# Kernel optimization log

Hardware: AMD Instinct MI355X
Metric: run time of the kernel (lower is better)

Reference implementation:

```python
import jax, jax.numpy as jnp
import numpy as np

D_MODEL = 128; D_STATE = 64; HEADDIM = 32; D_CONV = 4; EXPAND = 2
D_INNER = EXPAND * D_MODEL          # 256
NHEADS = D_INNER // HEADDIM         # 8
NGROUPS = 1
D_CONV_CH = D_INNER + 2 * NGROUPS * D_STATE      # 384
D_IN_PROJ = 2 * D_INNER + 2 * NGROUPS * D_STATE + NHEADS  # 648


def _mamba2(u, Win, convw, convb, dtb, Alog, Dp, normw, Wout):
    # u: (B, L, d_model). Mamba2 forward (ngroups=1, rmsnorm gated, no in/out bias).
    B, L, _ = u.shape
    zxbcdt = u @ Win                                   # (B,L,648)
    z, xBC, dt = jnp.split(zxbcdt, [D_INNER, D_INNER + D_CONV_CH], axis=-1)
    # depthwise causal conv1d (kernel D_CONV) + SiLU
    xp = jnp.pad(xBC, ((0, 0), (D_CONV - 1, 0), (0, 0)))
    xconv = sum(xp[:, k:k + L, :] * convw[k] for k in range(D_CONV)) + convb
    xBC = jax.nn.silu(xconv)
    x, Bm, Cm = jnp.split(xBC, [D_INNER, D_INNER + NGROUPS * D_STATE], axis=-1)
    dt = jax.nn.softplus(dt + dtb)                     # (B,L,H)
    A = -jnp.exp(Alog)                                 # (H,)
    xh = x.reshape(B, L, NHEADS, HEADDIM)              # (B,L,H,P)
    dA = jnp.exp(dt * A)                               # (B,L,H)

    def step(h, inp):
        dA_t, dt_t, B_t, C_t, x_t = inp
        h = h * dA_t[:, :, None, None] + jnp.einsum('bh,bn,bhp->bhpn', dt_t, B_t, x_t)
        y = jnp.einsum('bhpn,bn->bhp', h, C_t)
        return h, y

    h0 = jnp.zeros((B, NHEADS, HEADDIM, D_STATE), dtype=u.dtype)
    xs = (jnp.moveaxis(dA, 1, 0), jnp.moveaxis(dt, 1, 0), jnp.moveaxis(Bm, 1, 0),
          jnp.moveaxis(Cm, 1, 0), jnp.moveaxis(xh, 1, 0))
    _, ys = jax.lax.scan(step, h0, xs)
    y = jnp.moveaxis(ys, 0, 1) + Dp[None, None, :, None] * xh   # skip D
    y = y.reshape(B, L, D_INNER)
    # RMSNormGated (norm_before_gate=False): rmsnorm(y * silu(z)) * weight
    y = y * jax.nn.silu(z)
    y = y * jax.lax.rsqrt(jnp.mean(y * y, axis=-1, keepdims=True) + 1e-5) * normw
    return y @ Wout


def _cross_attn(x, ctx, Wq, bq, Wk, bk, Wv, bv, Wo, bo):
    Q = x @ Wq + bq
    K = ctx @ Wk + bk
    V = ctx @ Wv + bv
    att = jax.nn.softmax(jnp.einsum('bqd,bkd->bqk', Q, K) * (D_MODEL ** -0.5), axis=-1)
    return jnp.einsum('bqk,bkd->bqd', att, V) @ Wo + bo


def setup_inputs() -> dict:
    key = jax.random.key(0)
    ks = jax.random.split(key, 8)
    B, L = 2048, 8

    def lin(k, fi, fo):
        return jax.random.normal(k, (fi, fo), jnp.float32) / np.sqrt(fi)

    def mamba_params(kseq):
        k = jax.random.split(kseq, 6)
        dt = jax.random.uniform(k[3], (NHEADS,), minval=0.001, maxval=0.1)
        return {
            'Win': lin(k[0], D_MODEL, D_IN_PROJ),
            'convw': jax.random.normal(k[1], (D_CONV, D_CONV_CH), jnp.float32) * 0.2,
            'convb': jnp.zeros((D_CONV_CH,), jnp.float32),
            'dtb': dt + jnp.log(-jnp.expm1(-dt)),  # inverse softplus
            'Alog': jnp.log(jax.random.uniform(k[4], (NHEADS,), minval=1.0, maxval=16.0)),
            'D': jnp.ones((NHEADS,), jnp.float32),
            'normw': jnp.ones((D_INNER,), jnp.float32),
            'Wout': lin(k[5], D_INNER, D_MODEL),
        }

    inp = {
        'st_feature': jax.random.normal(ks[0], (B, L, D_MODEL), jnp.float32),
        'exp_feature': jax.random.normal(ks[1], (B, L, D_MODEL), jnp.float32),
    }
    for pref, p in (('st_', mamba_params(ks[2])), ('ex_', mamba_params(ks[3]))):
        for n, v in p.items():
            inp[pref + n] = v

    def ca(kseq, pref):
        k = jax.random.split(kseq, 4)
        d = {}
        for n, kk in zip(('Wq', 'Wk', 'Wv', 'Wo'), k):
            d[pref + n] = lin(kk, D_MODEL, D_MODEL)
            d[pref + 'b' + n[1]] = jnp.zeros((D_MODEL,), jnp.float32)
        return d

    inp.update(ca(ks[4], 'cx_'))  # cross_atten_exp
    inp.update(ca(ks[5], 'cs_'))  # cross_atten_st
    inp['mlp_W'] = lin(ks[6], 8 * 2 * D_MODEL, 1024)
    inp['mlp_b'] = jnp.zeros((1024,), jnp.float32)
    return inp


def reference(st_feature, exp_feature,
              st_Win, st_convw, st_convb, st_dtb, st_Alog, st_D, st_normw, st_Wout,
              ex_Win, ex_convw, ex_convb, ex_dtb, ex_Alog, ex_D, ex_normw, ex_Wout,
              cx_Wq, cx_bq, cx_Wk, cx_bk, cx_Wv, cx_bv, cx_Wo, cx_bo,
              cs_Wq, cs_bq, cs_Wk, cs_bk, cs_Wv, cs_bv, cs_Wo, cs_bo,
              mlp_W, mlp_b):
    exp_f = _mamba2(exp_feature, ex_Win, ex_convw, ex_convb, ex_dtb, ex_Alog, ex_D, ex_normw, ex_Wout)
    st_f = _mamba2(st_feature, st_Win, st_convw, st_convb, st_dtb, st_Alog, st_D, st_normw, st_Wout)
    exp_a = _cross_attn(exp_f, st_f, cx_Wq, cx_bq, cx_Wk, cx_bk, cx_Wv, cx_bv, cx_Wo, cx_bo)
    st_a = _cross_attn(st_f, exp_f, cs_Wq, cs_bq, cs_Wk, cs_bk, cs_Wv, cs_bv, cs_Wo, cs_bo)
    x = jnp.concatenate([st_a, exp_a], axis=-1)        # (B, 8, 256)
    x = x.reshape(x.shape[0], -1)                      # (B, 2048)
    return x @ mlp_W + mlp_b
```

## Files before the change

kernel.cpp:

```cpp
#include <hip/hip_runtime.h>
#include <hip/hip_bf16.h>
#include <math.h>

#define B_SZ 2048
#define L_SEQ 8
#define DMODEL 128
#define DSTATE 64
#define HEADDIM 32
#define DCONV 4
#define DINNER 256
#define NHEADS 8
#define DCONVCH 384
#define DINPROJ 648
#define NPAD 656

typedef short bf16x8 __attribute__((ext_vector_type(8)));
typedef float floatx4 __attribute__((ext_vector_type(4)));

__device__ __forceinline__ float siluf(float x) {
    return x / (1.f + expf(-x));
}
__device__ __forceinline__ float bf2f(unsigned short h) {
    unsigned int u = ((unsigned int)h) << 16;
    return __builtin_bit_cast(float, u);
}
__device__ __forceinline__ unsigned short f2bf(float f) {
    __hip_bfloat16 b = __float2bfloat16(f);
    return __builtin_bit_cast(unsigned short, b);
}
__device__ __forceinline__ void unpack8(bf16x8 v, float* o) {
    #pragma unroll
    for (int j = 0; j < 8; ++j) o[j] = bf2f((unsigned short)v[j]);
}
__device__ __forceinline__ void gl_lds16(const unsigned short* g, unsigned short* l) {
    __builtin_amdgcn_global_load_lds(
        (const __attribute__((address_space(1))) unsigned int*)g,
        (__attribute__((address_space(3))) unsigned int*)l, 16, 0, 0);
}

__global__ __launch_bounds__(256) void prep_weights(
    const float* __restrict__ st_Win, const float* __restrict__ ex_Win,
    const float* __restrict__ st_Wout, const float* __restrict__ ex_Wout,
    const float* __restrict__ cs_Wq, const float* __restrict__ cs_Wk,
    const float* __restrict__ cs_Wv, const float* __restrict__ cs_Wo,
    const float* __restrict__ cx_Wq, const float* __restrict__ cx_Wk,
    const float* __restrict__ cx_Wv, const float* __restrict__ cx_Wo,
    const float* __restrict__ mlp_W,
    unsigned short* __restrict__ winT_st, unsigned short* __restrict__ winT_ex,
    unsigned short* __restrict__ woutT_st, unsigned short* __restrict__ woutT_ex,
    unsigned short* __restrict__ attnWT, unsigned short* __restrict__ mlpWt)
{
    __shared__ float tile[32][33];
    int blk = blockIdx.x;
    if (blk < 656) {
        const float* src = blk < 328 ? st_Win : ex_Win;
        unsigned short* dst = blk < 328 ? winT_st : winT_ex;
        int idx = (blk % 328) * 256 + threadIdx.x;
        if (idx >= NPAD * 128) return;
        int n = idx / 128, k = idx % 128;
        float v = (n < DINPROJ) ? src[k * DINPROJ + n] : 0.f;
        dst[idx] = f2bf(v);
    } else if (blk < 912) {
        const float* src = blk < 784 ? st_Wout : ex_Wout;
        unsigned short* dst = blk < 784 ? woutT_st : woutT_ex;
        int idx = ((blk - 656) % 128) * 256 + threadIdx.x;
        int n = idx / 256, k = idx % 256;
        dst[idx] = f2bf(src[k * 128 + n]);
    } else if (blk < 1424) {
        int b2 = blk - 912;
        int mat = b2 >> 6;
        const float* src = mat == 0 ? cs_Wq : mat == 1 ? cs_Wk : mat == 2 ? cs_Wv :
                           mat == 3 ? cs_Wo : mat == 4 ? cx_Wq : mat == 5 ? cx_Wk :
                           mat == 6 ? cx_Wv : cx_Wo;
        int e = (b2 & 63) * 256 + threadIdx.x;
        int n = e >> 7, k = e & 127;
        attnWT[mat * 16384 + n * 128 + k] = f2bf(src[k * 128 + n]);
    } else {
        int b2 = blk - 1424;
        int n0 = (b2 & 31) * 32, k0 = (b2 >> 5) * 32;
        const int tid = threadIdx.x;
        const int c = tid & 31, r0 = tid >> 5;
        for (int rr = r0; rr < 32; rr += 8)
            tile[rr][c] = mlp_W[(size_t)(k0 + rr) * 1024 + n0 + c];
        __syncthreads();
        for (int rr = r0; rr < 32; rr += 8)
            mlpWt[(size_t)(n0 + rr) * 2048 + k0 + c] = f2bf(tile[c][rr]);
    }
}

#define LDK 136
#define LDZ 648
#define LDY 264
__global__ __launch_bounds__(256, 4) void mamba_dual(
    const float* __restrict__ u_ex, const float* __restrict__ u_st,
    const unsigned short* __restrict__ WinT_ex, const unsigned short* __restrict__ WinT_st,
    const float* __restrict__ convw_ex, const float* __restrict__ convw_st,
    const float* __restrict__ convb_ex, const float* __restrict__ convb_st,
    const float* __restrict__ dtb_ex, const float* __restrict__ dtb_st,
    const float* __restrict__ Alog_ex, const float* __restrict__ Alog_st,
    const float* __restrict__ Dp_ex, const float* __restrict__ Dp_st,
    const float* __restrict__ normw_ex, const float* __restrict__ normw_st,
    const unsigned short* __restrict__ WoutT_ex, const unsigned short* __restrict__ WoutT_st,
    unsigned short* __restrict__ out_ex, unsigned short* __restrict__ out_st)
{
    const int which = blockIdx.x >> 10;
    const float* u = which ? u_st : u_ex;
    const unsigned short* WinT = which ? WinT_st : WinT_ex;
    const float* convw = which ? convw_st : convw_ex;
    const float* convb = which ? convb_st : convb_ex;
    const float* dtb = which ? dtb_st : dtb_ex;
    const float* Alog = which ? Alog_st : Alog_ex;
    const float* Dp = which ? Dp_st : Dp_ex;
    const float* normw = which ? normw_st : normw_ex;
    const unsigned short* WoutT = which ? WoutT_st : WoutT_ex;
    unsigned short* outf = which ? out_st : out_ex;

    const int tid = threadIdx.x;
    const int lane = tid & 63;
    const int wave = tid >> 6;
    const int l15 = lane & 15;
    const int q8 = (lane >> 4) * 8;
    const int row0 = (lane >> 4) * 4;
    const int grow0 = (blockIdx.x & 1023) * 16;

    __shared__ __align__(16) unsigned short uA[16 * LDK];
    __shared__ __align__(16) unsigned short zx[16 * LDZ];
    __shared__ __align__(16) unsigned short yb[16 * LDY];
    __shared__ float dtraw[16][8];
    __shared__ float dtv[2][8][8];
    __shared__ float cum[2][8][8];
    __shared__ float Gm[2][8][8];
    __shared__ float red[16][32];
    __shared__ float rstd[16];
    float* coefp = (float*)uA;

    for (int i = tid; i < 512; i += 256) {
        int r = i >> 5, k4 = (i & 31) * 4;
        float4 v = *(const float4*)(u + (size_t)(grow0 + r) * DMODEL + k4);
        ushort4 h;
        h.x = f2bf(v.x); h.y = f2bf(v.y); h.z = f2bf(v.z); h.w = f2bf(v.w);
        *(ushort4*)(uA + r * LDK + k4) = h;
    }
    __syncthreads();

    {
        bf16x8 af[4];
        #pragma unroll
        for (int kk = 0; kk < 4; ++kk)
            af[kk] = *(const bf16x8*)(uA + l15 * LDK + kk * 32 + q8);
        for (int nt = wave; nt < 41; nt += 4) {
            floatx4 acc = {0.f, 0.f, 0.f, 0.f};
            const unsigned short* bp = WinT + (size_t)(nt * 16 + l15) * 128 + q8;
            #pragma unroll
            for (int kk = 0; kk < 4; ++kk) {
                bf16x8 bf = *(const bf16x8*)(bp + kk * 32);
                acc = __builtin_amdgcn_mfma_f32_16x16x32_bf16(af[kk], bf, acc, 0, 0, 0);
            }
            if (nt == 40) {
                if (l15 < 8) {
                    #pragma unroll
                    for (int r = 0; r < 4; ++r)
                        dtraw[row0 + r][l15] = acc[r];
                }
            } else {
                #pragma unroll
                for (int r = 0; r < 4; ++r)
                    zx[(row0 + r) * LDZ + nt * 16 + l15] = f2bf(acc[r]);
            }
        }
    }
    __syncthreads();

    float cv[3][8];
    {
        #pragma unroll
        for (int it = 0; it < 3; ++it) {
            int i = tid + it * 256;
            int r = i / 48, g = i % 48;
            int c0 = g * 8;
            int l = r & 7, bloc = r >> 3;
            float s[8];
            float4 cb0 = *(const float4*)(convb + c0);
            float4 cb1 = *(const float4*)(convb + c0 + 4);
            s[0] = cb0.x; s[1] = cb0.y; s[2] = cb0.z; s[3] = cb0.w;
            s[4] = cb1.x; s[5] = cb1.y; s[6] = cb1.z; s[7] = cb1.w;
            #pragma unroll
            for (int k = 0; k < DCONV; ++k) {
                int lp = l + k - (DCONV - 1);
                if (lp >= 0) {
                    bf16x8 v = *(const bf16x8*)(zx + (bloc * 8 + lp) * LDZ + 256 + c0);
                    float vf[8];
                    unpack8(v, vf);
                    float4 w0 = *(const float4*)(convw + k * DCONVCH + c0);
                    float4 w1 = *(const float4*)(convw + k * DCONVCH + c0 + 4);
                    s[0] += vf[0] * w0.x; s[1] += vf[1] * w0.y;
                    s[2] += vf[2] * w0.z; s[3] += vf[3] * w0.w;
                    s[4] += vf[4] * w1.x; s[5] += vf[5] * w1.y;
                    s[6] += vf[6] * w1.z; s[7] += vf[7] * w1.w;
                }
            }
            #pragma unroll
            for (int j = 0; j < 8; ++j) cv[it][j] = siluf(s[j]);
        }
        if (tid < 128) {
            int r = tid >> 3, h = tid & 7;
            float v = dtraw[r][h] + dtb[h];
            dtv[r >> 3][r & 7][h] = (v > 20.f) ? v : log1pf(expf(v));
        }
    }
    __syncthreads();
    {
        #pragma unroll
        for (int it = 0; it < 3; ++it) {
            int i = tid + it * 256;
            int r = i / 48, c0 = (i % 48) * 8;
            bf16x8 o;
            #pragma unroll
            for (int j = 0; j < 8; ++j) o[j] = (short)f2bf(cv[it][j]);
            *(bf16x8*)(zx + r * LDZ + 256 + c0) = o;
        }
    }
    __syncthreads();

    if (tid < 128) {
        int bloc = tid >> 6, t = (tid >> 3) & 7, s = tid & 7;
        float a = 0.f;
        #pragma unroll
        for (int n = 0; n < DSTATE; n += 8) {
            bf16x8 bv = *(const bf16x8*)(zx + (bloc * 8 + s) * LDZ + 512 + n);
            bf16x8 cvv = *(const bf16x8*)(zx + (bloc * 8 + t) * LDZ + 576 + n);
            float bf_[8], cf_[8];
            unpack8(bv, bf_); unpack8(cvv, cf_);
            #pragma unroll
            for (int j = 0; j < 8; ++j) a += bf_[j] * cf_[j];
        }
        Gm[bloc][t][s] = a;
    } else if (tid < 144) {
        int j = tid - 128;
        int bloc = j >> 3, h = j & 7;
        float c = 0.f;
        for (int l = 0; l < L_SEQ; ++l) { c += dtv[bloc][l][h]; cum[bloc][l][h] = c; }
    }
    __syncthreads();

    for (int i = tid; i < 1024; i += 256) {
        int bloc = i >> 9, t = (i >> 6) & 7, s = (i >> 3) & 7, h = i & 7;
        float A = -expf(Alog[h]);
        coefp[i] = (s <= t)
            ? Gm[bloc][t][s] * expf(A * (cum[bloc][t][h] - cum[bloc][s][h])) * dtv[bloc][s][h]
            : 0.f;
    }
    __syncthreads();

    {
        #pragma unroll
        for (int it = 0; it < 2; ++it) {
            int i = tid + it * 256;
            int r = i >> 5, g = i & 31;
            int c0 = g * 8, h = g >> 2;
            int bloc = r >> 3, t = r & 7;
            float acc[8];
            {
                bf16x8 xv = *(const bf16x8*)(zx + r * LDZ + 256 + c0);
                float xf[8]; unpack8(xv, xf);
                float d = Dp[h];
                #pragma unroll
                for (int j = 0; j < 8; ++j) acc[j] = d * xf[j];
            }
            for (int s = 0; s <= t; ++s) {
                float cf = coefp[((bloc * 8 + t) * 8 + s) * 8 + h];
                bf16x8 xv = *(const bf16x8*)(zx + (bloc * 8 + s) * LDZ + 256 + c0);
                float xf[8]; unpack8(xv, xf);
                #pragma unroll
                for (int j = 0; j < 8; ++j) acc[j] += cf * xf[j];
            }
            bf16x8 zv = *(const bf16x8*)(zx + r * LDZ + c0);
            float zf[8]; unpack8(zv, zf);
            float p = 0.f;
            bf16x8 o;
            #pragma unroll
            for (int j = 0; j < 8; ++j) {
                float y = acc[j] * siluf(zf[j]);
                p += y * y;
                o[j] = (short)f2bf(y);
            }
            *(bf16x8*)(yb + r * LDY + c0) = o;
            red[r][g] = p;
        }
    }
    __syncthreads();
    if (tid < 16) {
        float s = 0.f;
        #pragma unroll
        for (int j = 0; j < 32; ++j) s += red[tid][j];
        rstd[tid] = rsqrtf(s / (float)DINNER + 1e-5f);
    }
    __syncthreads();
    {
        #pragma unroll
        for (int it = 0; it < 2; ++it) {
            int i = tid + it * 256;
            int r = i >> 5, c0 = (i & 31) * 8;
            bf16x8 v = *(const bf16x8*)(yb + r * LDY + c0);
            float vf[8]; unpack8(v, vf);
            float4 w0 = *(const float4*)(normw + c0);
            float4 w1 = *(const float4*)(normw + c0 + 4);
            float rs = rstd[r];
            bf16x8 o;
            o[0] = (short)f2bf(vf[0] * rs * w0.x); o[1] = (short)f2bf(vf[1] * rs * w0.y);
            o[2] = (short)f2bf(vf[2] * rs * w0.z); o[3] = (short)f2bf(vf[3] * rs * w0.w);
            o[4] = (short)f2bf(vf[4] * rs * w1.x); o[5] = (short)f2bf(vf[5] * rs * w1.y);
            o[6] = (short)f2bf(vf[6] * rs * w1.z); o[7] = (short)f2bf(vf[7] * rs * w1.w);
            *(bf16x8*)(yb + r * LDY + c0) = o;
        }
    }
    __syncthreads();

    {
        bf16x8 af[8];
        #pragma unroll
        for (int kk = 0; kk < 8; ++kk)
            af[kk] = *(const bf16x8*)(yb + l15 * LDY + kk * 32 + q8);
        #pragma unroll
        for (int ni = 0; ni < 2; ++ni) {
            int nt = wave * 2 + ni;
            floatx4 acc = {0.f, 0.f, 0.f, 0.f};
            const unsigned short* bp = WoutT + (size_t)(nt * 16 + l15) * 256 + q8;
            #pragma unroll
            for (int kk = 0; kk < 8; ++kk) {
                bf16x8 bf = *(const bf16x8*)(bp + kk * 32);
                acc = __builtin_amdgcn_mfma_f32_16x16x32_bf16(af[kk], bf, acc, 0, 0, 0);
            }
            #pragma unroll
            for (int r = 0; r < 4; ++r)
                outf[(size_t)(grow0 + row0 + r) * DMODEL + nt * 16 + l15] = f2bf(acc[r]);
        }
    }
}

#define ASTR 136
#define VSTR 40
#define PSTR 40
__global__ __launch_bounds__(256, 2) void attn_kernel(
    const unsigned short* __restrict__ st_f,
    const unsigned short* __restrict__ exp_f,
    const unsigned short* __restrict__ WT,
    const float* __restrict__ cs_bq, const float* __restrict__ cs_bk,
    const float* __restrict__ cs_bv, const float* __restrict__ cs_bo,
    const float* __restrict__ cx_bq, const float* __restrict__ cx_bk,
    const float* __restrict__ cx_bv, const float* __restrict__ cx_bo,
    __hip_bfloat16* __restrict__ x)
{
    const int tid = threadIdx.x;
    const int lane = tid & 63, wave = tid >> 6;
    const int l15 = lane & 15;
    const int q8 = (lane >> 4) * 8;
    const int row0 = (lane >> 4) * 4;
    const int grow0 = blockIdx.x * 32;
    const int b0 = blockIdx.x * 4;
    const float scale = 0.08838834764831845f;

    __shared__ __align__(16) unsigned short stf[32 * ASTR];
    __shared__ __align__(16) unsigned short exf[32 * ASTR];
    __shared__ __align__(16) unsigned short Qs[32 * ASTR];
    __shared__ __align__(16) unsigned short Ks[32 * ASTR];
    __shared__ __align__(16) unsigned short attv[32 * ASTR];
    __shared__ __align__(16) unsigned short Vt[128 * VSTR];
    __shared__ __align__(16) unsigned short P[32 * PSTR];
    __shared__ float Ss[32][33];

    #pragma unroll
    for (int it = 0; it < 2; ++it) {
        int i = tid + it * 256;
        int r = i >> 4, c8 = (i & 15) * 8;
        *(uint4*)(stf + r * ASTR + c8) = *(const uint4*)(st_f + (size_t)(grow0 + r) * 128 + c8);
        *(uint4*)(exf + r * ASTR + c8) = *(const uint4*)(exp_f + (size_t)(grow0 + r) * 128 + c8);
    }
    __syncthreads();

    #pragma unroll
    for (int pass = 0; pass < 2; ++pass) {
        const unsigned short* qsrc = pass ? exf : stf;
        const unsigned short* kvsrc = pass ? stf : exf;
        const unsigned short* Wq = WT + (size_t)pass * 4 * 16384;
        const unsigned short* Wk = Wq + 16384;
        const unsigned short* Wv = Wq + 32768;
        const unsigned short* Wo = Wq + 49152;
        const float* bq = pass ? cx_bq : cs_bq;
        const float* bk = pass ? cx_bk : cs_bk;
        const float* bv = pass ? cx_bv : cs_bv;
        const float* bo = pass ? cx_bo : cs_bo;

        {
            bf16x8 aq[2][4], akv[2][4];
            #pragma unroll
            for (int mt = 0; mt < 2; ++mt)
                #pragma unroll
                for (int kk = 0; kk < 4; ++kk) {
                    aq[mt][kk]  = *(const bf16x8*)(qsrc  + (mt * 16 + l15) * ASTR + kk * 32 + q8);
                    akv[mt][kk] = *(const bf16x8*)(kvsrc + (mt * 16 + l15) * ASTR + kk * 32 + q8);
                }
            #pragma unroll
            for (int ni = 0; ni < 2; ++ni) {
                int nc = (wave * 2 + ni) * 16 + l15;
                floatx4 aq0 = {0,0,0,0}, aq1 = {0,0,0,0};
                floatx4 ak0 = {0,0,0,0}, ak1 = {0,0,0,0};
                floatx4 av0 = {0,0,0,0}, av1 = {0,0,0,0};
                #pragma unroll
                for (int kk = 0; kk < 4; ++kk) {
                    bf16x8 wqf = *(const bf16x8*)(Wq + (size_t)nc * 128 + kk * 32 + q8);
                    bf16x8 wkf = *(const bf16x8*)(Wk + (size_t)nc * 128 + kk * 32 + q8);
                    bf16x8 wvf = *(const bf16x8*)(Wv + (size_t)nc * 128 + kk * 32 + q8);
                    aq0 = __builtin_amdgcn_mfma_f32_16x16x32_bf16(aq[0][kk],  wqf, aq0, 0, 0, 0);
                    aq1 = __builtin_amdgcn_mfma_f32_16x16x32_bf16(aq[1][kk],  wqf, aq1, 0, 0, 0);
                    ak0 = __builtin_amdgcn_mfma_f32_16x16x32_bf16(akv[0][kk], wkf, ak0, 0, 0, 0);
                    ak1 = __builtin_amdgcn_mfma_f32_16x16x32_bf16(akv[1][kk], wkf, ak1, 0, 0, 0);
                    av0 = __builtin_amdgcn_mfma_f32_16x16x32_bf16(akv[0][kk], wvf, av0, 0, 0, 0);
                    av1 = __builtin_amdgcn_mfma_f32_16x16x32_bf16(akv[1][kk], wvf, av1, 0, 0, 0);
                }
                float bqv = bq[nc], bkv = bk[nc], bvv = bv[nc];
                #pragma unroll
                for (int r = 0; r < 4; ++r) {
                    Qs[(row0 + r) * ASTR + nc]      = f2bf(aq0[r] + bqv);
                    Qs[(16 + row0 + r) * ASTR + nc] = f2bf(aq1[r] + bqv);
                    Ks[(row0 + r) * ASTR + nc]      = f2bf(ak0[r] + bkv);
                    Ks[(16 + row0 + r) * ASTR + nc] = f2bf(ak1[r] + bkv);
                    Vt[nc * VSTR + row0 + r]        = f2bf(av0[r] + bvv);
                    Vt[nc * VSTR + 16 + row0 + r]   = f2bf(av1[r] + bvv);
                }
            }
        }
        __syncthreads();

        {
            int mtS = wave >> 1, ntS = wave & 1;
            floatx4 s = {0,0,0,0};
            #pragma unroll
            for (int kk = 0; kk < 4; ++kk) {
                bf16x8 a = *(const bf16x8*)(Qs + (mtS * 16 + l15) * ASTR + kk * 32 + q8);
                bf16x8 b = *(const bf16x8*)(Ks + (ntS * 16 + l15) * ASTR + kk * 32 + q8);
                s = __builtin_amdgcn_mfma_f32_16x16x32_bf16(a, b, s, 0, 0, 0);
            }
            #pragma unroll
            for (int r = 0; r < 4; ++r)
                Ss[mtS * 16 + row0 + r][ntS * 16 + l15] = s[r];
        }
        __syncthreads();

        if (tid < 32) {
            int r = tid, c0 = (r >> 3) * 8;
            float v[8], mx = -1e30f;
            #pragma unroll
            for (int c = 0; c < 8; ++c) {
                v[c] = Ss[r][c0 + c] * scale;
                mx = fmaxf(mx, v[c]);
            }
            float sum = 0.f;
            #pragma unroll
            for (int c = 0; c < 8; ++c) { v[c] = expf(v[c] - mx); sum += v[c]; }
            float inv = 1.f / sum;
            #pragma unroll
            for (int c = 0; c < 32; ++c) {
                float pv = (c >= c0 && c < c0 + 8) ? v[c - c0] * inv : 0.f;
                P[r * PSTR + c] = f2bf(pv);
            }
        }
        __syncthreads();

        {
            #pragma unroll
            for (int ni = 0; ni < 2; ++ni) {
                int nc = (wave * 2 + ni) * 16 + l15;
                bf16x8 bv_ = *(const bf16x8*)(Vt + nc * VSTR + q8);
                #pragma unroll
                for (int mt = 0; mt < 2; ++mt) {
                    bf16x8 ap = *(const bf16x8*)(P + (mt * 16 + l15) * PSTR + q8);
                    floatx4 o = {0,0,0,0};
                    o = __builtin_amdgcn_mfma_f32_16x16x32_bf16(ap, bv_, o, 0, 0, 0);
                    #pragma unroll
                    for (int r = 0; r < 4; ++r)
                        attv[(mt * 16 + row0 + r) * ASTR + nc] = f2bf(o[r]);
                }
            }
        }
        __syncthreads();

        {
            bf16x8 ao[2][4];
            #pragma unroll
            for (int mt = 0; mt < 2; ++mt)
                #pragma unroll
                for (int kk = 0; kk < 4; ++kk)
                    ao[mt][kk] = *(const bf16x8*)(attv + (mt * 16 + l15) * ASTR + kk * 32 + q8);
            #pragma unroll
            for (int ni = 0; ni < 2; ++ni) {
                int nc = (wave * 2 + ni) * 16 + l15;
                floatx4 a0 = {0,0,0,0}, a1 = {0,0,0,0};
                #pragma unroll
                for (int kk = 0; kk < 4; ++kk) {
                    bf16x8 wof = *(const bf16x8*)(Wo + (size_t)nc * 128 + kk * 32 + q8);
                    a0 = __builtin_amdgcn_mfma_f32_16x16x32_bf16(ao[0][kk], wof, a0, 0, 0, 0);
                    a1 = __builtin_amdgcn_mfma_f32_16x16x32_bf16(ao[1][kk], wof, a1, 0, 0, 0);
                }
                float bov = bo[nc];
                #pragma unroll
                for (int r = 0; r < 4; ++r) {
                    int rr0 = row0 + r;
                    int rr1 = 16 + row0 + r;
                    x[(size_t)(b0 + (rr0 >> 3)) * 2048 + (rr0 & 7) * 256 + pass * 128 + nc] =
                        __float2bfloat16(a0[r] + bov);
                    x[(size_t)(b0 + (rr1 >> 3)) * 2048 + (rr1 & 7) * 256 + pass * 128 + nc] =
                        __float2bfloat16(a1[r] + bov);
                }
            }
        }
        __syncthreads();
    }
}

__global__ __launch_bounds__(256, 2) void mlp_mfma(
    const unsigned short* __restrict__ X,
    const unsigned short* __restrict__ Wt,
    const float* __restrict__ bias,
    float* __restrict__ out)
{
    __shared__ __align__(16) unsigned short As[64 * 64];
    __shared__ __align__(16) unsigned short Bs[64 * 64];
    const int tid = threadIdx.x;
    const int wave = tid >> 6, lane = tid & 63;
    const int wm = (wave >> 1) * 32, wn = (wave & 1) * 32;
    const int bm = blockIdx.y * 64, bn = blockIdx.x * 64;
    const int l15 = lane & 15, q8 = (lane >> 4) * 8;

    const int c0i = tid, c1i = tid + 256;
    const int r0s = c0i >> 3, c0s = ((c0i & 7) ^ (r0s & 7)) * 8;
    const int r1s = c1i >> 3, c1s = ((c1i & 7) ^ (r1s & 7)) * 8;
    const unsigned short* gA0 = X + (size_t)(bm + r0s) * 2048 + c0s;
    const unsigned short* gA1 = X + (size_t)(bm + r1s) * 2048 + c1s;
    const unsigned short* gB0 = Wt + (size_t)(bn + r0s) * 2048 + c0s;
    const unsigned short* gB1 = Wt + (size_t)(bn + r1s) * 2048 + c1s;
    unsigned short* lA0 = As + c0i * 8;
    unsigned short* lA1 = As + c1i * 8;
    unsigned short* lB0 = Bs + c0i * 8;
    unsigned short* lB1 = Bs + c1i * 8;

    floatx4 acc[2][2];
    #pragma unroll
    for (int i = 0; i < 2; ++i)
        #pragma unroll
        for (int j = 0; j < 2; ++j) acc[i][j] = (floatx4){0.f, 0.f, 0.f, 0.f};

    const int ra0 = wm + l15, ra1 = wm + 16 + l15;
    const int rb0 = wn + l15, rb1 = wn + 16 + l15;

    for (int k0 = 0; k0 < 2048; k0 += 64) {
        __syncthreads();
        gl_lds16(gA0 + k0, lA0);
        gl_lds16(gA1 + k0, lA1);
        gl_lds16(gB0 + k0, lB0);
        gl_lds16(gB1 + k0, lB1);
        __syncthreads();
        #pragma unroll
        for (int ks = 0; ks < 2; ++ks) {
            int xx = ks * 4 + (q8 >> 3);
            bf16x8 a0 = *(const bf16x8*)(As + (ra0 * 8 + (xx ^ (ra0 & 7))) * 8);
            bf16x8 a1 = *(const bf16x8*)(As + (ra1 * 8 + (xx ^ (ra1 & 7))) * 8);
            bf16x8 b0 = *(const bf16x8*)(Bs + (rb0 * 8 + (xx ^ (rb0 & 7))) * 8);
            bf16x8 b1 = *(const bf16x8*)(Bs + (rb1 * 8 + (xx ^ (rb1 & 7))) * 8);
            acc[0][0] = __builtin_amdgcn_mfma_f32_16x16x32_bf16(a0, b0, acc[0][0], 0, 0, 0);
            acc[0][1] = __builtin_amdgcn_mfma_f32_16x16x32_bf16(a0, b1, acc[0][1], 0, 0, 0);
            acc[1][0] = __builtin_amdgcn_mfma_f32_16x16x32_bf16(a1, b0, acc[1][0], 0, 0, 0);
            acc[1][1] = __builtin_amdgcn_mfma_f32_16x16x32_bf16(a1, b1, acc[1][1], 0, 0, 0);
        }
    }

    const int row0 = (lane >> 4) * 4;
    #pragma unroll
    for (int j = 0; j < 2; ++j) {
        int col = bn + wn + j * 16 + l15;
        float bv = bias[col];
        #pragma unroll
        for (int r = 0; r < 4; ++r) {
            out[(size_t)(bm + wm + row0 + r) * 1024 + col] = acc[0][j][r] + bv;
            out[(size_t)(bm + wm + 16 + row0 + r) * 1024 + col] = acc[1][j][r] + bv;
        }
    }
}

extern "C" void kernel_launch(void* const* d_in, const int* in_sizes, int n_in,
                              void* d_out, int out_size, void* d_ws, size_t ws_size,
                              hipStream_t stream) {
    const float* st_feature = (const float*)d_in[0];
    const float* exp_feature = (const float*)d_in[1];
    const float* st_Win = (const float*)d_in[2];
    const float* st_convw = (const float*)d_in[3];
    const float* st_convb = (const float*)d_in[4];
    const float* st_dtb = (const float*)d_in[5];
    const float* st_Alog = (const float*)d_in[6];
    const float* st_D = (const float*)d_in[7];
    const float* st_normw = (const float*)d_in[8];
    const float* st_Wout = (const float*)d_in[9];
    const float* ex_Win = (const float*)d_in[10];
    const float* ex_convw = (const float*)d_in[11];
    const float* ex_convb = (const float*)d_in[12];
    const float* ex_dtb = (const float*)d_in[13];
    const float* ex_Alog = (const float*)d_in[14];
    const float* ex_D = (const float*)d_in[15];
    const float* ex_normw = (const float*)d_in[16];
    const float* ex_Wout = (const float*)d_in[17];
    const float* cx_Wq = (const float*)d_in[18]; const float* cx_bq = (const float*)d_in[19];
    const float* cx_Wk = (const float*)d_in[20]; const float* cx_bk = (const float*)d_in[21];
    const float* cx_Wv = (const float*)d_in[22]; const float* cx_bv = (const float*)d_in[23];
    const float* cx_Wo = (const float*)d_in[24]; const float* cx_bo = (const float*)d_in[25];
    const float* cs_Wq = (const float*)d_in[26]; const float* cs_bq = (const float*)d_in[27];
    const float* cs_Wk = (const float*)d_in[28]; const float* cs_bk = (const float*)d_in[29];
    const float* cs_Wv = (const float*)d_in[30]; const float* cs_bv = (const float*)d_in[31];
    const float* cs_Wo = (const float*)d_in[32]; const float* cs_bo = (const float*)d_in[33];
    const float* mlp_W = (const float*)d_in[34];
    const float* mlp_b = (const float*)d_in[35];

    unsigned short* wsu = (unsigned short*)d_ws;
    unsigned short* st_fb  = wsu;
    unsigned short* exp_fb = st_fb + (size_t)B_SZ * L_SEQ * DMODEL;
    unsigned short* xbuf   = exp_fb + (size_t)B_SZ * L_SEQ * DMODEL;
    unsigned short* wtbuf  = xbuf + (size_t)2048 * 2048;
    unsigned short* winT_st = wtbuf + (size_t)1024 * 2048;
    unsigned short* winT_ex = winT_st + (size_t)NPAD * 128;
    unsigned short* woutT_st = winT_ex + (size_t)NPAD * 128;
    unsigned short* woutT_ex = woutT_st + (size_t)128 * 256;
    unsigned short* attnWT  = woutT_ex + (size_t)128 * 256;

    prep_weights<<<3472, 256, 0, stream>>>(
        st_Win, ex_Win, st_Wout, ex_Wout,
        cs_Wq, cs_Wk, cs_Wv, cs_Wo, cx_Wq, cx_Wk, cx_Wv, cx_Wo, mlp_W,
        winT_st, winT_ex, woutT_st, woutT_ex, attnWT, wtbuf);
    mamba_dual<<<2048, 256, 0, stream>>>(
        exp_feature, st_feature, winT_ex, winT_st,
        ex_convw, st_convw, ex_convb, st_convb,
        ex_dtb, st_dtb, ex_Alog, st_Alog, ex_D, st_D,
        ex_normw, st_normw, woutT_ex, woutT_st,
        exp_fb, st_fb);
    attn_kernel<<<B_SZ / 4, 256, 0, stream>>>(st_fb, exp_fb, attnWT,
                                              cs_bq, cs_bk, cs_bv, cs_bo,
                                              cx_bq, cx_bk, cx_bv, cx_bo,
                                              (__hip_bfloat16*)xbuf);
    {
        dim3 g(1024 / 64, 2048 / 64);
        mlp_mfma<<<g, 256, 0, stream>>>(xbuf, wtbuf, mlp_b, (float*)d_out);
    }
}
```

Before: 255.5 us.

## Fold RMSNorm weight into Wout, shuffle-reduce rstd, double-buffer MLP GEMM

The RMSNorm weight is folded into the transposed Wout during weight prep, and the per-row rstd is applied after the output projection. This removes the separate normalization pass and its LDS buffers, and the row sum of squares is reduced with wave shuffles instead of an LDS reduction. Softplus for dt moves into the in-projection epilogue. The MLP GEMM gets a double-buffered LDS pipeline so global-to-LDS loads overlap the MFMAs, and the occupancy hints of both kernels are raised. Multiplying by rstd after the projection, instead of before bf16 rounding, slightly changes numerics.

```diff
diff --git a/kernel.cpp b/kernel.cpp
--- a/kernel.cpp
+++ b/kernel.cpp
@@ -41,6 +41,7 @@
 __global__ __launch_bounds__(256) void prep_weights(
     const float* __restrict__ st_Win, const float* __restrict__ ex_Win,
     const float* __restrict__ st_Wout, const float* __restrict__ ex_Wout,
+    const float* __restrict__ st_normw, const float* __restrict__ ex_normw,
     const float* __restrict__ cs_Wq, const float* __restrict__ cs_Wk,
     const float* __restrict__ cs_Wv, const float* __restrict__ cs_Wo,
     const float* __restrict__ cx_Wq, const float* __restrict__ cx_Wk,
@@ -62,10 +63,11 @@
         dst[idx] = f2bf(v);
     } else if (blk < 912) {
         const float* src = blk < 784 ? st_Wout : ex_Wout;
+        const float* nw  = blk < 784 ? st_normw : ex_normw;
         unsigned short* dst = blk < 784 ? woutT_st : woutT_ex;
         int idx = ((blk - 656) % 128) * 256 + threadIdx.x;
         int n = idx / 256, k = idx % 256;
-        dst[idx] = f2bf(src[k * 128 + n]);
+        dst[idx] = f2bf(src[k * 128 + n] * nw[k]);
     } else if (blk < 1424) {
         int b2 = blk - 912;
         int mat = b2 >> 6;
@@ -90,8 +92,7 @@
 
 #define LDK 136
 #define LDZ 648
-#define LDY 264
-__global__ __launch_bounds__(256, 4) void mamba_dual(
+__global__ __launch_bounds__(256, 6) void mamba_dual(
     const float* __restrict__ u_ex, const float* __restrict__ u_st,
     const unsigned short* __restrict__ WinT_ex, const unsigned short* __restrict__ WinT_st,
     const float* __restrict__ convw_ex, const float* __restrict__ convw_st,
@@ -99,7 +100,6 @@
     const float* __restrict__ dtb_ex, const float* __restrict__ dtb_st,
     const float* __restrict__ Alog_ex, const float* __restrict__ Alog_st,
     const float* __restrict__ Dp_ex, const float* __restrict__ Dp_st,
-    const float* __restrict__ normw_ex, const float* __restrict__ normw_st,
     const unsigned short* __restrict__ WoutT_ex, const unsigned short* __restrict__ WoutT_st,
     unsigned short* __restrict__ out_ex, unsigned short* __restrict__ out_st)
 {
@@ -111,7 +111,6 @@
     const float* dtb = which ? dtb_st : dtb_ex;
     const float* Alog = which ? Alog_st : Alog_ex;
     const float* Dp = which ? Dp_st : Dp_ex;
-    const float* normw = which ? normw_st : normw_ex;
     const unsigned short* WoutT = which ? WoutT_st : WoutT_ex;
     unsigned short* outf = which ? out_st : out_ex;
 
@@ -125,14 +124,11 @@
 
     __shared__ __align__(16) unsigned short uA[16 * LDK];
     __shared__ __align__(16) unsigned short zx[16 * LDZ];
-    __shared__ __align__(16) unsigned short yb[16 * LDY];
-    __shared__ float dtraw[16][8];
     __shared__ float dtv[2][8][8];
     __shared__ float cum[2][8][8];
     __shared__ float Gm[2][8][8];
-    __shared__ float red[16][32];
-    __shared__ float rstd[16];
     float* coefp = (float*)uA;
+    float* rstdp = coefp + 1024;
 
     for (int i = tid; i < 512; i += 256) {
         int r = i >> 5, k4 = (i & 31) * 4;
@@ -158,9 +154,13 @@
             }
             if (nt == 40) {
                 if (l15 < 8) {
+                    float dbv = dtb[l15];
                     #pragma unroll
-                    for (int r = 0; r < 4; ++r)
-                        dtraw[row0 + r][l15] = acc[r];
+                    for (int r = 0; r < 4; ++r) {
+                        int rr = row0 + r;
+                        float v = acc[r] + dbv;
+                        dtv[rr >> 3][rr & 7][l15] = (v > 20.f) ? v : log1pf(expf(v));
+                    }
                 }
             } else {
                 #pragma unroll
@@ -202,11 +202,6 @@
             #pragma unroll
             for (int j = 0; j < 8; ++j) cv[it][j] = siluf(s[j]);
         }
-        if (tid < 128) {
-            int r = tid >> 3, h = tid & 7;
-            float v = dtraw[r][h] + dtb[h];
-            dtv[r >> 3][r & 7][h] = (v > 20.f) ? v : log1pf(expf(v));
-        }
     }
     __syncthreads();
     {
@@ -252,6 +247,9 @@
     }
     __syncthreads();
 
+    float pj[2];
+    bf16x8 yo[2];
+    int rF[2], c0F[2];
     {
         #pragma unroll
         for (int it = 0; it < 2; ++it) {
@@ -277,50 +275,37 @@
             bf16x8 zv = *(const bf16x8*)(zx + r * LDZ + c0);
             float zf[8]; unpack8(zv, zf);
             float p = 0.f;
-            bf16x8 o;
             #pragma unroll
             for (int j = 0; j < 8; ++j) {
                 float y = acc[j] * siluf(zf[j]);
                 p += y * y;
-                o[j] = (short)f2bf(y);
-            }
-            *(bf16x8*)(yb + r * LDY + c0) = o;
-            red[r][g] = p;
-        }
-    }
-    __syncthreads();
-    if (tid < 16) {
-        float s = 0.f;
-        #pragma unroll
-        for (int j = 0; j < 32; ++j) s += red[tid][j];
-        rstd[tid] = rsqrtf(s / (float)DINNER + 1e-5f);
-    }
-    __syncthreads();
-    {
-        #pragma unroll
-        for (int it = 0; it < 2; ++it) {
-            int i = tid + it * 256;
-            int r = i >> 5, c0 = (i & 31) * 8;
-            bf16x8 v = *(const bf16x8*)(yb + r * LDY + c0);
-            float vf[8]; unpack8(v, vf);
-            float4 w0 = *(const float4*)(normw + c0);
-            float4 w1 = *(const float4*)(normw + c0 + 4);
-            float rs = rstd[r];
-            bf16x8 o;
-            o[0] = (short)f2bf(vf[0] * rs * w0.x); o[1] = (short)f2bf(vf[1] * rs * w0.y);
-            o[2] = (short)f2bf(vf[2] * rs * w0.z); o[3] = (short)f2bf(vf[3] * rs * w0.w);
-            o[4] = (short)f2bf(vf[4] * rs * w1.x); o[5] = (short)f2bf(vf[5] * rs * w1.y);
-            o[6] = (short)f2bf(vf[6] * rs * w1.z); o[7] = (short)f2bf(vf[7] * rs * w1.w);
-            *(bf16x8*)(yb + r * LDY + c0) = o;
-        }
-    }
+                yo[it][j] = (short)f2bf(y);
+            }
+            pj[it] = p; rF[it] = r; c0F[it] = c0;
+        }
+    }
+    #pragma unroll
+    for (int m = 1; m < 32; m <<= 1) {
+        pj[0] += __shfl_xor(pj[0], m);
+        pj[1] += __shfl_xor(pj[1], m);
+    }
+    if ((tid & 31) == 0) {
+        rstdp[rF[0]] = rsqrtf(pj[0] * (1.f / 256.f) + 1e-5f);
+        rstdp[rF[1]] = rsqrtf(pj[1] * (1.f / 256.f) + 1e-5f);
+    }
+    __syncthreads();
+    *(bf16x8*)(zx + rF[0] * LDZ + 256 + c0F[0]) = yo[0];
+    *(bf16x8*)(zx + rF[1] * LDZ + 256 + c0F[1]) = yo[1];
     __syncthreads();
 
     {
         bf16x8 af[8];
         #pragma unroll
         for (int kk = 0; kk < 8; ++kk)
-            af[kk] = *(const bf16x8*)(yb + l15 * LDY + kk * 32 + q8);
+            af[kk] = *(const bf16x8*)(zx + l15 * LDZ + 256 + kk * 32 + q8);
+        float rs[4];
+        #pragma unroll
+        for (int r = 0; r < 4; ++r) rs[r] = rstdp[row0 + r];
         #pragma unroll
         for (int ni = 0; ni < 2; ++ni) {
             int nt = wave * 2 + ni;
@@ -333,7 +318,7 @@
             }
             #pragma unroll
             for (int r = 0; r < 4; ++r)
-                outf[(size_t)(grow0 + row0 + r) * DMODEL + nt * 16 + l15] = f2bf(acc[r]);
+                outf[(size_t)(grow0 + row0 + r) * DMODEL + nt * 16 + l15] = f2bf(acc[r] * rs[r]);
         }
     }
 }
@@ -518,14 +503,14 @@
     }
 }
 
-__global__ __launch_bounds__(256, 2) void mlp_mfma(
+__global__ __launch_bounds__(256, 5) void mlp_mfma(
     const unsigned short* __restrict__ X,
     const unsigned short* __restrict__ Wt,
     const float* __restrict__ bias,
     float* __restrict__ out)
 {
-    __shared__ __align__(16) unsigned short As[64 * 64];
-    __shared__ __align__(16) unsigned short Bs[64 * 64];
+    __shared__ __align__(16) unsigned short As[2][64 * 64];
+    __shared__ __align__(16) unsigned short Bs[2][64 * 64];
     const int tid = threadIdx.x;
     const int wave = tid >> 6, lane = tid & 63;
     const int wm = (wave >> 1) * 32, wn = (wave & 1) * 32;
@@ -539,10 +524,6 @@
     const unsigned short* gA1 = X + (size_t)(bm + r1s) * 2048 + c1s;
     const unsigned short* gB0 = Wt + (size_t)(bn + r0s) * 2048 + c0s;
     const unsigned short* gB1 = Wt + (size_t)(bn + r1s) * 2048 + c1s;
-    unsigned short* lA0 = As + c0i * 8;
-    unsigned short* lA1 = As + c1i * 8;
-    unsigned short* lB0 = Bs + c0i * 8;
-    unsigned short* lB1 = Bs + c1i * 8;
 
     floatx4 acc[2][2];
     #pragma unroll
@@ -553,25 +534,39 @@
     const int ra0 = wm + l15, ra1 = wm + 16 + l15;
     const int rb0 = wn + l15, rb1 = wn + 16 + l15;
 
-    for (int k0 = 0; k0 < 2048; k0 += 64) {
-        __syncthreads();
-        gl_lds16(gA0 + k0, lA0);
-        gl_lds16(gA1 + k0, lA1);
-        gl_lds16(gB0 + k0, lB0);
-        gl_lds16(gB1 + k0, lB1);
-        __syncthreads();
+    gl_lds16(gA0, As[0] + c0i * 8);
+    gl_lds16(gA1, As[0] + c1i * 8);
+    gl_lds16(gB0, Bs[0] + c0i * 8);
+    gl_lds16(gB1, Bs[0] + c1i * 8);
+    __syncthreads();
+
+    int cur = 0;
+    for (int t = 0; t < 32; ++t) {
+        if (t < 31) {
+            int k0 = (t + 1) * 64;
+            unsigned short* An = As[cur ^ 1];
+            unsigned short* Bn = Bs[cur ^ 1];
+            gl_lds16(gA0 + k0, An + c0i * 8);
+            gl_lds16(gA1 + k0, An + c1i * 8);
+            gl_lds16(gB0 + k0, Bn + c0i * 8);
+            gl_lds16(gB1 + k0, Bn + c1i * 8);
+        }
+        const unsigned short* Ac = As[cur];
+        const unsigned short* Bc = Bs[cur];
         #pragma unroll
         for (int ks = 0; ks < 2; ++ks) {
             int xx = ks * 4 + (q8 >> 3);
-            bf16x8 a0 = *(const bf16x8*)(As + (ra0 * 8 + (xx ^ (ra0 & 7))) * 8);
-            bf16x8 a1 = *(const bf16x8*)(As + (ra1 * 8 + (xx ^ (ra1 & 7))) * 8);
-            bf16x8 b0 = *(const bf16x8*)(Bs + (rb0 * 8 + (xx ^ (rb0 & 7))) * 8);
-            bf16x8 b1 = *(const bf16x8*)(Bs + (rb1 * 8 + (xx ^ (rb1 & 7))) * 8);
+            bf16x8 a0 = *(const bf16x8*)(Ac + (ra0 * 8 + (xx ^ (ra0 & 7))) * 8);
+            bf16x8 a1 = *(const bf16x8*)(Ac + (ra1 * 8 + (xx ^ (ra1 & 7))) * 8);
+            bf16x8 b0 = *(const bf16x8*)(Bc + (rb0 * 8 + (xx ^ (rb0 & 7))) * 8);
+            bf16x8 b1 = *(const bf16x8*)(Bc + (rb1 * 8 + (xx ^ (rb1 & 7))) * 8);
             acc[0][0] = __builtin_amdgcn_mfma_f32_16x16x32_bf16(a0, b0, acc[0][0], 0, 0, 0);
             acc[0][1] = __builtin_amdgcn_mfma_f32_16x16x32_bf16(a0, b1, acc[0][1], 0, 0, 0);
             acc[1][0] = __builtin_amdgcn_mfma_f32_16x16x32_bf16(a1, b0, acc[1][0], 0, 0, 0);
             acc[1][1] = __builtin_amdgcn_mfma_f32_16x16x32_bf16(a1, b1, acc[1][1], 0, 0, 0);
         }
+        __syncthreads();
+        cur ^= 1;
     }
 
     const int row0 = (lane >> 4) * 4;
@@ -631,14 +626,14 @@
     unsigned short* attnWT  = woutT_ex + (size_t)128 * 256;
 
     prep_weights<<<3472, 256, 0, stream>>>(
-        st_Win, ex_Win, st_Wout, ex_Wout,
+        st_Win, ex_Win, st_Wout, ex_Wout, st_normw, ex_normw,
         cs_Wq, cs_Wk, cs_Wv, cs_Wo, cx_Wq, cx_Wk, cx_Wv, cx_Wo, mlp_W,
         winT_st, winT_ex, woutT_st, woutT_ex, attnWT, wtbuf);
     mamba_dual<<<2048, 256, 0, stream>>>(
         exp_feature, st_feature, winT_ex, winT_st,
         ex_convw, st_convw, ex_convb, st_convb,
         ex_dtb, st_dtb, ex_Alog, st_Alog, ex_D, st_D,
-        ex_normw, st_normw, woutT_ex, woutT_st,
+        woutT_ex, woutT_st,
         exp_fb, st_fb);
     attn_kernel<<<B_SZ / 4, 256, 0, stream>>>(st_fb, exp_fb, attnWT,
                                               cs_bq, cs_bk, cs_bv, cs_bo,
```

Measured after the change: 262.9 us. +2.9%, slower.
